# Optimization experiments

Hardware: AMD Instinct MI355X
Metric: run time of the kernel (lower is better)

The kernel has to match this reference:

```python
import jax, jax.numpy as jnp
import numpy as np

NUM_GROUPS = 32
EPS = 1e-5


def group_norm(x, w, b):
    # x: [B,C,H,W], 32 groups
    B, C, H, W = x.shape
    xg = x.reshape(B, NUM_GROUPS, C // NUM_GROUPS, H, W)
    mean = xg.mean(axis=(2, 3, 4), keepdims=True)
    var = xg.var(axis=(2, 3, 4), keepdims=True)
    xn = ((xg - mean) * jax.lax.rsqrt(var + EPS)).reshape(B, C, H, W)
    return xn * w[None, :, None, None] + b[None, :, None, None]


def conv1x1(x, w, b):
    # x: [B,C,H,W], w: [O,C], b: [O]
    return jnp.einsum('bchw,oc->bohw', x, w) + b[None, :, None, None]


def setup_inputs() -> dict:
    key = jax.random.key(0)
    ks = jax.random.split(key, 7)
    B, C, H, W = 16, 512, 32, 32
    x = jax.random.normal(ks[0], (B, C, H, W), dtype=jnp.float32)
    gn_w = jnp.ones((C,), dtype=jnp.float32)
    gn_b = jnp.zeros((C,), dtype=jnp.float32)
    s = 1.0 / np.sqrt(C)
    qkv_w = jax.random.normal(ks[1], (3 * C, C), dtype=jnp.float32) * s
    qkv_b = jnp.zeros((3 * C,), dtype=jnp.float32)
    proj_w = jax.random.normal(ks[2], (C, C), dtype=jnp.float32) * s
    proj_b = jnp.zeros((C,), dtype=jnp.float32)
    return {"x": x, "gn_w": gn_w, "gn_b": gn_b, "qkv_w": qkv_w,
            "qkv_b": qkv_b, "proj_w": proj_w, "proj_b": proj_b}


def reference(x, gn_w, gn_b, qkv_w, qkv_b, proj_w, proj_b):
    B, C, H, W = x.shape
    qkv = conv1x1(group_norm(x, gn_w, gn_b), qkv_w, qkv_b)
    q, k, v = jnp.split(qkv, 3, axis=1)
    scale = (C // 8) ** (-0.5)
    # attn: [B, h, w, H, W]
    attn = jnp.einsum('bchw,bcHW->bhwHW', q * scale, k)
    # NOTE: faithful to original torch code: softmax over the LAST axis only
    attn = jax.nn.softmax(attn, axis=-1)
    out = jnp.einsum('bhwHW,bcHW->bchw', attn, v)
    return x + conv1x1(out, proj_w, proj_b)
```

## Files before the change

### kernel.cpp

```cpp
#include <hip/hip_runtime.h>
#include <hip/hip_bf16.h>

#define B_    16
#define C_    512
#define S_    1024
#define NGRP  32
#define CPG   16

typedef __attribute__((ext_vector_type(8))) short  short8;
typedef __attribute__((ext_vector_type(4))) short  short4v;
typedef __attribute__((ext_vector_type(4))) float  floatx4;

__device__ __forceinline__ unsigned short f2bf(float f) {
    __hip_bfloat16 h = __float2bfloat16(f);
    unsigned short u;
    __builtin_memcpy(&u, &h, 2);
    return u;
}

__global__ __launch_bounds__(256)
void gn_fused_kernel(const float* __restrict__ x, const float* __restrict__ w,
                     const float* __restrict__ bias, __hip_bfloat16* __restrict__ xnT) {
    int bg = blockIdx.x;
    int b = bg >> 5, g = bg & 31;
    const float4* xp = (const float4*)(x + (size_t)bg * (CPG * S_));
    int tid = threadIdx.x;

    float4 vv[16];
    float s = 0.f, ss = 0.f;
#pragma unroll
    for (int r = 0; r < 16; ++r) {
        float4 v = xp[r * 256 + tid];
        vv[r] = v;
        s  += v.x + v.y + v.z + v.w;
        ss += v.x*v.x + v.y*v.y + v.z*v.z + v.w*v.w;
    }
    for (int off = 32; off > 0; off >>= 1) {
        s  += __shfl_down(s, off);
        ss += __shfl_down(ss, off);
    }
    __shared__ float red[2][4];
    __shared__ float msh[2];
    int wid = tid >> 6, lane = tid & 63;
    if (lane == 0) { red[0][wid] = s; red[1][wid] = ss; }
    __syncthreads();
    if (tid == 0) {
        float a = 0.f, c = 0.f;
        for (int i = 0; i < 4; ++i) { a += red[0][i]; c += red[1][i]; }
        float mean = a / (float)(CPG * S_);
        float var  = c / (float)(CPG * S_) - mean * mean;
        msh[0] = mean;
        msh[1] = rsqrtf(var + 1e-5f);
    }
    __syncthreads();
    float mean = msh[0], inv = msh[1];

    float sc[16], sh[16];
#pragma unroll
    for (int c = 0; c < 16; ++c) {
        float wc = w[g * 16 + c];
        sc[c] = inv * wc;
        sh[c] = bias[g * 16 + c] - mean * inv * wc;
    }

#pragma unroll
    for (int kk = 0; kk < 4; ++kk) {
        unsigned short outp[16];
#pragma unroll
        for (int c = 0; c < 16; ++c) {
            float v = (kk == 0) ? vv[c].x : (kk == 1) ? vv[c].y : (kk == 2) ? vv[c].z : vv[c].w;
            outp[c] = f2bf(v * sc[c] + sh[c]);
        }
        int srow = 4 * tid + kk;
        unsigned short* dst = (unsigned short*)xnT + ((size_t)(b * S_ + srow) * C_ + g * 16);
        *(short8*)dst       = *(short8*)outp;
        *(short8*)(dst + 8) = *(short8*)(outp + 8);
    }
}

__global__ __launch_bounds__(256)
void prep_kernel(const float* __restrict__ qkv_w, const float* __restrict__ proj_w,
                 const float* __restrict__ qkv_b,
                 unsigned short* __restrict__ bufX,
                 unsigned short* __restrict__ bufY,
                 float* __restrict__ bqWk, float* __restrict__ biasvp)
{
    int blk = blockIdx.x;
    int tid = threadIdx.x;
    if (blk < 192) {
        __shared__ float T[64][65];
        int mat = blk >> 6, tile = blk & 63;
        int r0 = (tile >> 3) * 64, c0 = (tile & 7) * 64;
        const float* src; unsigned short* dst;
        if (mat == 0)      { src = qkv_w + 512 * 512;  dst = bufX; }
        else if (mat == 1) { src = qkv_w;              dst = bufY; }
        else               { src = qkv_w + 1024 * 512; dst = bufY + 262144; }
#pragma unroll
        for (int rr = 0; rr < 4; ++rr) {
            int sr = rr * 16 + (tid >> 4);
            int sc = (tid & 15) * 4;
            float4 v = *(const float4*)(src + (size_t)(c0 + sr) * 512 + r0 + sc);
            T[sc][sr] = v.x; T[sc + 1][sr] = v.y; T[sc + 2][sr] = v.z; T[sc + 3][sr] = v.w;
        }
        __syncthreads();
#pragma unroll
        for (int rr = 0; rr < 4; ++rr) {
            int dr = rr * 16 + (tid >> 4);
            int dc = (tid & 15) * 4;
            short4v o;
            o[0] = (short)f2bf(T[dr][dc]);     o[1] = (short)f2bf(T[dr][dc + 1]);
            o[2] = (short)f2bf(T[dr][dc + 2]); o[3] = (short)f2bf(T[dr][dc + 3]);
            *(short4v*)(dst + (size_t)(r0 + dr) * 512 + c0 + dc) = o;
        }
    } else if (blk < 256) {
        unsigned short* wp = bufX + 262144;
#pragma unroll
        for (int t = 0; t < 4; ++t) {
            int i = (blk - 192) * 4096 + t * 1024 + tid * 4;
            float4 v = *(const float4*)(proj_w + i);
            short4v o;
            o[0] = (short)f2bf(v.x); o[1] = (short)f2bf(v.y);
            o[2] = (short)f2bf(v.z); o[3] = (short)f2bf(v.w);
            *(short4v*)(wp + i) = o;
        }
    } else if (blk < 264) {
        int sub = blk - 256;
        int j = (sub & 1) * 256 + tid;
        int o0 = (sub >> 1) * 128;
        float acc = 0.f;
#pragma unroll 8
        for (int oo = 0; oo < 128; ++oo) {
            int o = o0 + oo;
            acc += qkv_b[o] * qkv_w[(size_t)(512 + o) * 512 + j];
        }
        atomicAdd(&bqWk[j], acc);
    } else {
        int wv = tid >> 6, lane = tid & 63;
        int c = (blk - 264) * 4 + wv;
        float s = 0.f;
#pragma unroll
        for (int t = 0; t < 8; ++t)
            s += proj_w[(size_t)c * 512 + t * 64 + lane] * qkv_b[1024 + t * 64 + lane];
        for (int off = 32; off > 0; off >>= 1) s += __shfl_down(s, off);
        if (lane == 0) biasvp[c] = s;
    }
}

template<int BIAS_MODE, bool OUT_BF16, bool RESID, bool SWIZ, int KTOT>
__global__ __launch_bounds__(256)
void mfma_gemm(const unsigned short* __restrict__ A, const unsigned short* __restrict__ Bm,
               const float* __restrict__ bias, const float* __restrict__ resid,
               void* __restrict__ Yv,
               int lda, int ldb, int ldy,
               size_t sA, size_t sB, size_t sY, size_t sR, float alpha,
               int ntsh, int nxsh)
{
    __shared__ unsigned short As[2 * 128 * 32];
    __shared__ unsigned short Bs[2 * 128 * 32];
    int bx, by, bz;
    if (SWIZ) {
        int lin = blockIdx.x;
        int xcd = lin & 7, sup = lin >> 3;
        bz = xcd + ((sup >> ntsh) << 3);
        int tile = sup & ((1 << ntsh) - 1);
        bx = tile & ((1 << nxsh) - 1);
        by = tile >> nxsh;
    } else { bx = blockIdx.x; by = blockIdx.y; bz = blockIdx.z; }

    const unsigned short* Ab = A  + (size_t)bz * sA;
    const unsigned short* Bb = Bm + (size_t)bz * sB;
    const int tid = threadIdx.x, wave = tid >> 6, lane = tid & 63;
    const int m0 = by * 128, n0 = bx * 128;
    const int wr = wave >> 1, wc = wave & 1, lr = lane & 15, kq = lane >> 4;
    const int row0 = tid >> 2, kc0 = (tid & 3) << 3;

    floatx4 acc[4][4] = {};

    for (int k0 = 0; k0 < KTOT; k0 += 64) {
        __syncthreads();
#pragma unroll
        for (int kk = 0; kk < 2; ++kk) {
#pragma unroll
            for (int r = 0; r < 2; ++r) {
                const unsigned short* ga = Ab + (size_t)(m0 + r * 64 + row0) * lda + k0 + kk * 32 + kc0;
                __builtin_amdgcn_global_load_lds(
                    (const __attribute__((address_space(1))) void*)ga,
                    (__attribute__((address_space(3))) void*)(As + kk * 4096 + (r * 256 + wave * 64) * 8),
                    16, 0, 0);
                const unsigned short* gb = Bb + (size_t)(n0 + r * 64 + row0) * ldb + k0 + kk * 32 + kc0;
                __builtin_amdgcn_global_load_lds(
                    (const __attribute__((address_space(1))) void*)gb,
                    (__attribute__((address_space(3))) void*)(Bs + kk * 4096 + (r * 256 + wave * 64) * 8),
                    16, 0, 0);
            }
        }
        __syncthreads();

#pragma unroll
        for (int kk = 0; kk < 2; ++kk) {
            short8 af[4], bfr[4];
#pragma unroll
            for (int i = 0; i < 4; ++i)
                af[i] = *(const short8*)&As[kk * 4096 + (wr * 64 + i * 16 + lr) * 32 + kq * 8];
#pragma unroll
            for (int j = 0; j < 4; ++j)
                bfr[j] = *(const short8*)&Bs[kk * 4096 + (wc * 64 + j * 16 + lr) * 32 + kq * 8];
#pragma unroll
            for (int i = 0; i < 4; ++i)
#pragma unroll
                for (int j = 0; j < 4; ++j)
                    acc[i][j] = __builtin_amdgcn_mfma_f32_16x16x32_bf16(af[i], bfr[j], acc[i][j], 0, 0, 0);
        }
    }

    const size_t ybase = (size_t)bz * sY;
    const size_t rbase = (size_t)bz * sR;
#pragma unroll
    for (int i = 0; i < 4; ++i) {
#pragma unroll
        for (int r = 0; r < 4; ++r) {
            int m = m0 + wr * 64 + i * 16 + kq * 4 + r;
            float bm = (BIAS_MODE == 1) ? bias[m] : 0.f;
#pragma unroll
            for (int j = 0; j < 4; ++j) {
                int n = n0 + wc * 64 + j * 16 + lr;
                float vv = acc[i][j][r] * alpha + bm;
                if (BIAS_MODE == 2) vv += bias[n];
                if (RESID) vv += resid[rbase + (size_t)m * ldy + n];
                if (OUT_BF16)
                    ((__hip_bfloat16*)Yv)[ybase + (size_t)m * ldy + n] = __float2bfloat16(vv);
                else
                    ((float*)Yv)[ybase + (size_t)m * ldy + n] = vv;
            }
        }
    }
}

__global__ __launch_bounds__(512)
void scores_softmax8(const unsigned short* __restrict__ A,
                     const unsigned short* __restrict__ Bm,
                     unsigned short* __restrict__ P)
{
    __shared__ __align__(16) unsigned short lds[65536];
    char* asb = (char*)lds;
    char* bsb = (char*)lds + 65536;

    const int bid = blockIdx.x;
    const int bz = bid >> 4, t16 = bid & 15;
    const int by = t16 >> 2, bx = t16 & 3;
    const int m0 = by << 8, n0 = bx << 8;

    const size_t sAB = (size_t)S_ * 512;
    const unsigned short* Ab = A  + (size_t)bz * sAB;
    const unsigned short* Bb = Bm + (size_t)bz * sAB;

    const int tid = threadIdx.x, wave = tid >> 6, lane = tid & 63;
    const int wr = wave >> 2, wc = wave & 3;
    const int lr = lane & 15, kq = lane >> 4;
    const int swz = (lr & 7) << 4;

    floatx4 acc[8][4] = {};
    short8 aF[4][2], bF[2][2][2];

    auto stage = [&](const unsigned short* __restrict__ G, int row0, int t,
                     char* base, int buf, int half) {
#pragma unroll
        for (int c = 0; c < 2; ++c) {
            int x = c * 8192 + tid * 16;
            int row = x >> 7;
            int colb = (x & 127) ^ ((row & 7) << 4);
            const unsigned short* ga = G + (((size_t)(row0 + row)) << 9) + (t << 6) + (colb >> 1);
            char* ldst = base + buf * 32768 + half * 16384 + c * 8192 + wave * 1024;
            __builtin_amdgcn_global_load_lds(
                (const __attribute__((address_space(1))) void*)ga,
                (__attribute__((address_space(3))) void*)ldst, 16, 0, 0);
        }
    };
    auto rdA = [&](int buf, int mh, int ii, int kk) {
        int byte = buf * 32768 + wr * 16384 + (mh * 64 + ii * 16 + lr) * 128
                 + ((kk * 64 + kq * 16) ^ swz);
        return *(const short8*)(asb + byte);
    };
    auto rdB = [&](int buf, int nh, int jj, int kk) {
        int trow = wc * 64 + (nh * 2 + jj) * 16 + lr;
        int byte = buf * 32768 + (trow >> 7) * 16384 + (trow & 127) * 128
                 + ((kk * 64 + kq * 16) ^ swz);
        return *(const short8*)(bsb + byte);
    };

    stage(Ab, m0,       0, asb, 0, 0);
    stage(Bb, n0,       0, bsb, 0, 0);
    stage(Bb, n0 + 128, 0, bsb, 0, 1);
    stage(Ab, m0 + 128, 0, asb, 0, 1);
    stage(Ab, m0,       1, asb, 1, 0);
    stage(Bb, n0,       1, bsb, 1, 0);
    stage(Bb, n0 + 128, 1, bsb, 1, 1);
    asm volatile("s_waitcnt vmcnt(6)" ::: "memory");
    __builtin_amdgcn_s_barrier();

    for (int t = 0; t < 8; ++t) {
        const int buf = t & 1;
#pragma unroll
        for (int ii = 0; ii < 4; ++ii) { aF[ii][0] = rdA(buf, 0, ii, 0); aF[ii][1] = rdA(buf, 0, ii, 1); }
#pragma unroll
        for (int jj = 0; jj < 2; ++jj) { bF[0][jj][0] = rdB(buf, 0, jj, 0); bF[0][jj][1] = rdB(buf, 0, jj, 1); }
        if (t < 7) stage(Ab, m0 + 128, t + 1, asb, (t + 1) & 1, 1);
        __builtin_amdgcn_s_barrier();
        asm volatile("s_waitcnt lgkmcnt(0)" ::: "memory");
        __builtin_amdgcn_s_setprio(1);
#pragma unroll
        for (int ii = 0; ii < 4; ++ii)
#pragma unroll
            for (int jj = 0; jj < 2; ++jj)
#pragma unroll
                for (int kk = 0; kk < 2; ++kk)
                    acc[ii][jj] = __builtin_amdgcn_mfma_f32_16x16x32_bf16(aF[ii][kk], bF[0][jj][kk], acc[ii][jj], 0, 0, 0);
        __builtin_amdgcn_s_setprio(0);
        __builtin_amdgcn_s_barrier();
#pragma unroll
        for (int jj = 0; jj < 2; ++jj) { bF[1][jj][0] = rdB(buf, 1, jj, 0); bF[1][jj][1] = rdB(buf, 1, jj, 1); }
        __builtin_amdgcn_s_barrier();
        asm volatile("s_waitcnt lgkmcnt(0)" ::: "memory");
        __builtin_amdgcn_s_setprio(1);
#pragma unroll
        for (int ii = 0; ii < 4; ++ii)
#pragma unroll
            for (int jj = 0; jj < 2; ++jj)
#pragma unroll
                for (int kk = 0; kk < 2; ++kk)
                    acc[ii][2 + jj] = __builtin_amdgcn_mfma_f32_16x16x32_bf16(aF[ii][kk], bF[1][jj][kk], acc[ii][2 + jj], 0, 0, 0);
        __builtin_amdgcn_s_setprio(0);
        __builtin_amdgcn_s_barrier();
#pragma unroll
        for (int ii = 0; ii < 4; ++ii) { aF[ii][0] = rdA(buf, 1, ii, 0); aF[ii][1] = rdA(buf, 1, ii, 1); }
        if (t < 6) stage(Bb, n0, t + 2, bsb, buf, 0);
        __builtin_amdgcn_s_barrier();
        asm volatile("s_waitcnt lgkmcnt(0)" ::: "memory");
        __builtin_amdgcn_s_setprio(1);
#pragma unroll
        for (int ii = 0; ii < 4; ++ii)
#pragma unroll
            for (int jj = 0; jj < 2; ++jj)
#pragma unroll
                for (int kk = 0; kk < 2; ++kk)
                    acc[4 + ii][2 + jj] = __builtin_amdgcn_mfma_f32_16x16x32_bf16(aF[ii][kk], bF[1][jj][kk], acc[4 + ii][2 + jj], 0, 0, 0);
        __builtin_amdgcn_s_setprio(0);
        __builtin_amdgcn_s_barrier();
        if (t < 6) {
            stage(Ab, m0,       t + 2, asb, buf, 0);
            stage(Bb, n0 + 128, t + 2, bsb, buf, 1);
        }
        __builtin_amdgcn_s_setprio(1);
#pragma unroll
        for (int ii = 0; ii < 4; ++ii)
#pragma unroll
            for (int jj = 0; jj < 2; ++jj)
#pragma unroll
                for (int kk = 0; kk < 2; ++kk)
                    acc[4 + ii][jj] = __builtin_amdgcn_mfma_f32_16x16x32_bf16(aF[ii][kk], bF[0][jj][kk], acc[4 + ii][jj], 0, 0, 0);
        __builtin_amdgcn_s_setprio(0);
        if (t < 6) { asm volatile("s_waitcnt vmcnt(6)" ::: "memory"); }
        else       { asm volatile("s_waitcnt vmcnt(0)" ::: "memory"); }
        __builtin_amdgcn_s_barrier();
    }

#pragma unroll
    for (int j = 0; j < 4; ++j) {
        int sqc = wc * 64 + j * 16 + lr;
        int srow = sqc * 512;
        int sxor = (sqc & 7) << 4;
#pragma unroll
        for (int h = 0; h < 4; ++h) {
            float v0[4], v1[4];
            float mx = -1e30f;
#pragma unroll
            for (int r = 0; r < 4; ++r) {
                v0[r] = acc[2 * h][j][r]     * 0.125f;
                v1[r] = acc[2 * h + 1][j][r] * 0.125f;
                mx = fmaxf(mx, fmaxf(v0[r], v1[r]));
            }
            mx = fmaxf(mx, __shfl_xor(mx, 16));
            mx = fmaxf(mx, __shfl_xor(mx, 32));
            float sm = 0.f;
#pragma unroll
            for (int r = 0; r < 4; ++r) {
                v0[r] = __expf(v0[r] - mx);
                v1[r] = __expf(v1[r] - mx);
                sm += v0[r] + v1[r];
            }
            sm += __shfl_xor(sm, 16);
            sm += __shfl_xor(sm, 32);
            float inv = 1.f / sm;
            short4v p0, p1;
#pragma unroll
            for (int r = 0; r < 4; ++r) {
                p0[r] = (short)f2bf(v0[r] * inv);
                p1[r] = (short)f2bf(v1[r] * inv);
            }
            int kb = (wr * 128 + h * 32 + kq * 4) * 2;
            *(short4v*)(asb + ((srow + kb) ^ sxor))      = p0;
            *(short4v*)(asb + ((srow + kb + 32) ^ sxor)) = p1;
        }
    }
    __syncthreads();

    const size_t pbase = ((size_t)bz << 20) + (size_t)n0 * 1024 + m0;
#pragma unroll
    for (int it = 0; it < 16; ++it) {
        int row = wave * 32 + it * 2 + (lane >> 5);
        int colb = (lane & 31) << 4;
        short8 v = *(const short8*)(asb + ((row * 512 + colb) ^ ((row & 7) << 4)));
        *(short8*)(P + pbase + (size_t)row * 1024 + (colb >> 1)) = v;
    }
}

extern "C" void kernel_launch(void* const* d_in, const int* in_sizes, int n_in,
                              void* d_out, int out_size, void* d_ws, size_t ws_size,
                              hipStream_t stream) {
    const float* x     = (const float*)d_in[0];
    const float* gn_w  = (const float*)d_in[1];
    const float* gn_b  = (const float*)d_in[2];
    const float* qkv_w = (const float*)d_in[3];
    const float* qkv_b = (const float*)d_in[4];
    const float* pr_w  = (const float*)d_in[5];
    const float* pr_b  = (const float*)d_in[6];
    float* out = (float*)d_out;

    char* w = (char*)d_ws;
    __hip_bfloat16* xnT  = (__hip_bfloat16*)w;
    __hip_bfloat16* u    = (__hip_bfloat16*)(w + (16u << 20));
    __hip_bfloat16* Vp   = (__hip_bfloat16*)(w + (32u << 20));
    __hip_bfloat16* P    = (__hip_bfloat16*)(w + (48u << 20));
    unsigned short* bufX = (unsigned short*)(w + (80u << 20));
    unsigned short* bufY = (unsigned short*)(w + (81u << 20));
    unsigned short* bufZ = (unsigned short*)(w + (82u << 20));
    float*          bqWk = (float*)(w + (83u << 20));
    float*          bvp  = (float*)(w + (83u << 20) + 4096);

    hipMemsetAsync(bqWk, 0, 512 * sizeof(float), stream);

    prep_kernel<<<392, 256, 0, stream>>>(qkv_w, pr_w, qkv_b, bufX, bufY, bqWk, bvp);

    gn_fused_kernel<<<B_ * NGRP, 256, 0, stream>>>(x, gn_w, gn_b, xnT);

    mfma_gemm<0, true, false, false, 512><<<dim3(4, 4, 2), 256, 0, stream>>>(
        bufX, bufY, nullptr, nullptr, bufZ,
        512, 512, 512, 262144, 262144, 262144, 0, 1.f, 0, 0);

    mfma_gemm<2, true, false, false, 512><<<dim3(4, 128, 1), 256, 0, stream>>>(
        (const unsigned short*)xnT, bufZ, bqWk, nullptr, u,
        512, 512, 512, 0, 0, 0, 0, 1.f, 0, 0);

    mfma_gemm<1, true, false, true, 512><<<512, 256, 0, stream>>>(
        bufZ + 262144, (const unsigned short*)xnT, bvp, nullptr, Vp,
        512, 512, 1024, 0, (size_t)S_ * 512, (size_t)512 * S_, 0, 1.f, 5, 3);

    scores_softmax8<<<256, 512, 0, stream>>>(
        (const unsigned short*)xnT, (const unsigned short*)u, (unsigned short*)P);

    mfma_gemm<1, false, true, true, 1024><<<512, 256, 0, stream>>>(
        (const unsigned short*)Vp, (const unsigned short*)P, pr_b, x, out,
        1024, 1024, 1024, (size_t)512 * S_, (size_t)S_ * S_, (size_t)512 * S_,
        (size_t)512 * S_, 1.f, 5, 3);
}
```

Baseline: 209.6 us.

## Fuse attention scores, softmax and PV-projection GEMM; merge GN with weight GEMM

```diff
diff --git a/kernel.cpp b/kernel.cpp
--- a/kernel.cpp
+++ b/kernel.cpp
@@ -11,71 +11,15 @@
 typedef __attribute__((ext_vector_type(4))) short  short4v;
 typedef __attribute__((ext_vector_type(4))) float  floatx4;
 
+#define GLOAD16(ga, ld) __builtin_amdgcn_global_load_lds( \
+    (const __attribute__((address_space(1))) void*)(ga),  \
+    (__attribute__((address_space(3))) void*)(ld), 16, 0, 0)
+
 __device__ __forceinline__ unsigned short f2bf(float f) {
     __hip_bfloat16 h = __float2bfloat16(f);
     unsigned short u;
     __builtin_memcpy(&u, &h, 2);
     return u;
-}
-
-__global__ __launch_bounds__(256)
-void gn_fused_kernel(const float* __restrict__ x, const float* __restrict__ w,
-                     const float* __restrict__ bias, __hip_bfloat16* __restrict__ xnT) {
-    int bg = blockIdx.x;
-    int b = bg >> 5, g = bg & 31;
-    const float4* xp = (const float4*)(x + (size_t)bg * (CPG * S_));
-    int tid = threadIdx.x;
-
-    float4 vv[16];
-    float s = 0.f, ss = 0.f;
-#pragma unroll
-    for (int r = 0; r < 16; ++r) {
-        float4 v = xp[r * 256 + tid];
-        vv[r] = v;
-        s  += v.x + v.y + v.z + v.w;
-        ss += v.x*v.x + v.y*v.y + v.z*v.z + v.w*v.w;
-    }
-    for (int off = 32; off > 0; off >>= 1) {
-        s  += __shfl_down(s, off);
-        ss += __shfl_down(ss, off);
-    }
-    __shared__ float red[2][4];
-    __shared__ float msh[2];
-    int wid = tid >> 6, lane = tid & 63;
-    if (lane == 0) { red[0][wid] = s; red[1][wid] = ss; }
-    __syncthreads();
-    if (tid == 0) {
-        float a = 0.f, c = 0.f;
-        for (int i = 0; i < 4; ++i) { a += red[0][i]; c += red[1][i]; }
-        float mean = a / (float)(CPG * S_);
-        float var  = c / (float)(CPG * S_) - mean * mean;
-        msh[0] = mean;
-        msh[1] = rsqrtf(var + 1e-5f);
-    }
-    __syncthreads();
-    float mean = msh[0], inv = msh[1];
-
-    float sc[16], sh[16];
-#pragma unroll
-    for (int c = 0; c < 16; ++c) {
-        float wc = w[g * 16 + c];
-        sc[c] = inv * wc;
-        sh[c] = bias[g * 16 + c] - mean * inv * wc;
-    }
-
-#pragma unroll
-    for (int kk = 0; kk < 4; ++kk) {
-        unsigned short outp[16];
-#pragma unroll
-        for (int c = 0; c < 16; ++c) {
-            float v = (kk == 0) ? vv[c].x : (kk == 1) ? vv[c].y : (kk == 2) ? vv[c].z : vv[c].w;
-            outp[c] = f2bf(v * sc[c] + sh[c]);
-        }
-        int srow = 4 * tid + kk;
-        unsigned short* dst = (unsigned short*)xnT + ((size_t)(b * S_ + srow) * C_ + g * 16);
-        *(short8*)dst       = *(short8*)outp;
-        *(short8*)(dst + 8) = *(short8*)(outp + 8);
-    }
 }
 
 __global__ __launch_bounds__(256)
@@ -146,113 +90,136 @@
     }
 }
 
-template<int BIAS_MODE, bool OUT_BF16, bool RESID, bool SWIZ, int KTOT>
 __global__ __launch_bounds__(256)
-void mfma_gemm(const unsigned short* __restrict__ A, const unsigned short* __restrict__ Bm,
-               const float* __restrict__ bias, const float* __restrict__ resid,
-               void* __restrict__ Yv,
-               int lda, int ldb, int ldy,
-               size_t sA, size_t sB, size_t sY, size_t sR, float alpha,
-               int ntsh, int nxsh)
+void gn_plus_w(const float* __restrict__ x, const float* __restrict__ gnw,
+               const float* __restrict__ gnb, __hip_bfloat16* __restrict__ xnT,
+               const unsigned short* __restrict__ bufX,
+               const unsigned short* __restrict__ bufY,
+               unsigned short* __restrict__ bufZ)
 {
-    __shared__ unsigned short As[2 * 128 * 32];
-    __shared__ unsigned short Bs[2 * 128 * 32];
-    int bx, by, bz;
-    if (SWIZ) {
-        int lin = blockIdx.x;
-        int xcd = lin & 7, sup = lin >> 3;
-        bz = xcd + ((sup >> ntsh) << 3);
-        int tile = sup & ((1 << ntsh) - 1);
-        bx = tile & ((1 << nxsh) - 1);
-        by = tile >> nxsh;
-    } else { bx = blockIdx.x; by = blockIdx.y; bz = blockIdx.z; }
-
-    const unsigned short* Ab = A  + (size_t)bz * sA;
-    const unsigned short* Bb = Bm + (size_t)bz * sB;
-    const int tid = threadIdx.x, wave = tid >> 6, lane = tid & 63;
-    const int m0 = by * 128, n0 = bx * 128;
-    const int wr = wave >> 1, wc = wave & 1, lr = lane & 15, kq = lane >> 4;
-    const int row0 = tid >> 2, kc0 = (tid & 3) << 3;
-
-    floatx4 acc[4][4] = {};
-
-    for (int k0 = 0; k0 < KTOT; k0 += 64) {
+    __shared__ __align__(16) char smem[32832];
+    int blk = blockIdx.x;
+    int tid = threadIdx.x;
+
+    if (blk < 512) {
+        int b = blk >> 5, g = blk & 31;
+        const float4* xp = (const float4*)(x + (size_t)blk * (CPG * S_));
+        float4 vv[16];
+        float s = 0.f, ss = 0.f;
+#pragma unroll
+        for (int r = 0; r < 16; ++r) {
+            float4 v = xp[r * 256 + tid];
+            vv[r] = v;
+            s  += v.x + v.y + v.z + v.w;
+            ss += v.x*v.x + v.y*v.y + v.z*v.z + v.w*v.w;
+        }
+        for (int off = 32; off > 0; off >>= 1) {
+            s  += __shfl_down(s, off);
+            ss += __shfl_down(ss, off);
+        }
+        float* red = (float*)(smem + 32768);
+        float* msh = (float*)(smem + 32800);
+        int wid = tid >> 6, lane = tid & 63;
+        if (lane == 0) { red[wid] = s; red[4 + wid] = ss; }
         __syncthreads();
-#pragma unroll
-        for (int kk = 0; kk < 2; ++kk) {
-#pragma unroll
-            for (int r = 0; r < 2; ++r) {
-                const unsigned short* ga = Ab + (size_t)(m0 + r * 64 + row0) * lda + k0 + kk * 32 + kc0;
-                __builtin_amdgcn_global_load_lds(
-                    (const __attribute__((address_space(1))) void*)ga,
-                    (__attribute__((address_space(3))) void*)(As + kk * 4096 + (r * 256 + wave * 64) * 8),
-                    16, 0, 0);
-                const unsigned short* gb = Bb + (size_t)(n0 + r * 64 + row0) * ldb + k0 + kk * 32 + kc0;
-                __builtin_amdgcn_global_load_lds(
-                    (const __attribute__((address_space(1))) void*)gb,
-                    (__attribute__((address_space(3))) void*)(Bs + kk * 4096 + (r * 256 + wave * 64) * 8),
-                    16, 0, 0);
-            }
+        if (tid == 0) {
+            float a = 0.f, c = 0.f;
+            for (int i = 0; i < 4; ++i) { a += red[i]; c += red[4 + i]; }
+            float mean = a / (float)(CPG * S_);
+            float var  = c / (float)(CPG * S_) - mean * mean;
+            msh[0] = mean;
+            msh[1] = rsqrtf(var + 1e-5f);
         }
         __syncthreads();
-
-#pragma unroll
-        for (int kk = 0; kk < 2; ++kk) {
-            short8 af[4], bfr[4];
-#pragma unroll
-            for (int i = 0; i < 4; ++i)
-                af[i] = *(const short8*)&As[kk * 4096 + (wr * 64 + i * 16 + lr) * 32 + kq * 8];
-#pragma unroll
-            for (int j = 0; j < 4; ++j)
-                bfr[j] = *(const short8*)&Bs[kk * 4096 + (wc * 64 + j * 16 + lr) * 32 + kq * 8];
-#pragma unroll
-            for (int i = 0; i < 4; ++i)
+        float mean = msh[0], inv = msh[1];
+
+        float sc[16], sh[16];
+#pragma unroll
+        for (int c = 0; c < 16; ++c) {
+            float wc = gnw[g * 16 + c];
+            sc[c] = inv * wc;
+            sh[c] = gnb[g * 16 + c] - mean * inv * wc;
+        }
+#pragma unroll
+        for (int kk = 0; kk < 4; ++kk) {
+            unsigned short outp[16];
+#pragma unroll
+            for (int c = 0; c < 16; ++c) {
+                float v = (kk == 0) ? vv[c].x : (kk == 1) ? vv[c].y : (kk == 2) ? vv[c].z : vv[c].w;
+                outp[c] = f2bf(v * sc[c] + sh[c]);
+            }
+            int srow = 4 * tid + kk;
+            unsigned short* dst = (unsigned short*)xnT + ((size_t)(b * S_ + srow) * C_ + g * 16);
+            *(short8*)dst       = *(short8*)outp;
+            *(short8*)(dst + 8) = *(short8*)(outp + 8);
+        }
+    } else {
+        unsigned short* As = (unsigned short*)smem;
+        unsigned short* Bs = (unsigned short*)(smem + 16384);
+        int id = blk - 512;
+        int bx = id & 3, by = (id >> 2) & 3, bz = id >> 4;
+        const unsigned short* Ab = bufX + (size_t)bz * 262144;
+        const unsigned short* Bb = bufY + (size_t)bz * 262144;
+        __hip_bfloat16* Y = (__hip_bfloat16*)bufZ + (size_t)bz * 262144;
+        const int wave = tid >> 6, lane = tid & 63;
+        const int m0 = by * 128, n0 = bx * 128;
+        const int wr = wave >> 1, wc = wave & 1, lr = lane & 15, kq = lane >> 4;
+        const int row0 = tid >> 2, kc0 = (tid & 3) << 3;
+
+        floatx4 acc[4][4] = {};
+        for (int k0 = 0; k0 < 512; k0 += 64) {
+            __syncthreads();
+#pragma unroll
+            for (int kk = 0; kk < 2; ++kk) {
+#pragma unroll
+                for (int r = 0; r < 2; ++r) {
+                    const unsigned short* ga = Ab + (size_t)(m0 + r * 64 + row0) * 512 + k0 + kk * 32 + kc0;
+                    GLOAD16(ga, As + kk * 4096 + (r * 256 + wave * 64) * 8);
+                    const unsigned short* gb = Bb + (size_t)(n0 + r * 64 + row0) * 512 + k0 + kk * 32 + kc0;
+                    GLOAD16(gb, Bs + kk * 4096 + (r * 256 + wave * 64) * 8);
+                }
+            }
+            __syncthreads();
+#pragma unroll
+            for (int kk = 0; kk < 2; ++kk) {
+                short8 af[4], bfr[4];
+#pragma unroll
+                for (int i = 0; i < 4; ++i)
+                    af[i] = *(const short8*)&As[kk * 4096 + (wr * 64 + i * 16 + lr) * 32 + kq * 8];
 #pragma unroll
                 for (int j = 0; j < 4; ++j)
-                    acc[i][j] = __builtin_amdgcn_mfma_f32_16x16x32_bf16(af[i], bfr[j], acc[i][j], 0, 0, 0);
-        }
+                    bfr[j] = *(const short8*)&Bs[kk * 4096 + (wc * 64 + j * 16 + lr) * 32 + kq * 8];
+#pragma unroll
+                for (int i = 0; i < 4; ++i)
+#pragma unroll
+                    for (int j = 0; j < 4; ++j)
+                        acc[i][j] = __builtin_amdgcn_mfma_f32_16x16x32_bf16(af[i], bfr[j], acc[i][j], 0, 0, 0);
+            }
+        }
+#pragma unroll
+        for (int i = 0; i < 4; ++i)
+#pragma unroll
+            for (int r = 0; r < 4; ++r) {
+                int m = m0 + wr * 64 + i * 16 + kq * 4 + r;
+#pragma unroll
+                for (int j = 0; j < 4; ++j) {
+                    int n = n0 + wc * 64 + j * 16 + lr;
+                    Y[(size_t)m * 512 + n] = __float2bfloat16(acc[i][j][r]);
+                }
+            }
     }
-
-    const size_t ybase = (size_t)bz * sY;
-    const size_t rbase = (size_t)bz * sR;
-#pragma unroll
-    for (int i = 0; i < 4; ++i) {
-#pragma unroll
-        for (int r = 0; r < 4; ++r) {
-            int m = m0 + wr * 64 + i * 16 + kq * 4 + r;
-            float bm = (BIAS_MODE == 1) ? bias[m] : 0.f;
-#pragma unroll
-            for (int j = 0; j < 4; ++j) {
-                int n = n0 + wc * 64 + j * 16 + lr;
-                float vv = acc[i][j][r] * alpha + bm;
-                if (BIAS_MODE == 2) vv += bias[n];
-                if (RESID) vv += resid[rbase + (size_t)m * ldy + n];
-                if (OUT_BF16)
-                    ((__hip_bfloat16*)Yv)[ybase + (size_t)m * ldy + n] = __float2bfloat16(vv);
-                else
-                    ((float*)Yv)[ybase + (size_t)m * ldy + n] = vv;
-            }
-        }
-    }
-}
-
-__global__ __launch_bounds__(512)
-void scores_softmax8(const unsigned short* __restrict__ A,
-                     const unsigned short* __restrict__ Bm,
-                     unsigned short* __restrict__ P)
+}
+
+template<int BIAS_MODE>
+__device__ __forceinline__
+void gemm256_body(char* lds, const unsigned short* __restrict__ Ab,
+                  const unsigned short* __restrict__ Bb,
+                  const float* __restrict__ bias,
+                  __hip_bfloat16* __restrict__ Y,
+                  int ldy, size_t ybase, int m0, int n0)
 {
-    __shared__ __align__(16) unsigned short lds[65536];
-    char* asb = (char*)lds;
-    char* bsb = (char*)lds + 65536;
-
-    const int bid = blockIdx.x;
-    const int bz = bid >> 4, t16 = bid & 15;
-    const int by = t16 >> 2, bx = t16 & 3;
-    const int m0 = by << 8, n0 = bx << 8;
-
-    const size_t sAB = (size_t)S_ * 512;
-    const unsigned short* Ab = A  + (size_t)bz * sAB;
-    const unsigned short* Bb = Bm + (size_t)bz * sAB;
+    char* asb = lds;
+    char* bsb = lds + 65536;
 
     const int tid = threadIdx.x, wave = tid >> 6, lane = tid & 63;
     const int wr = wave >> 2, wc = wave & 3;
@@ -270,10 +237,7 @@
             int row = x >> 7;
             int colb = (x & 127) ^ ((row & 7) << 4);
             const unsigned short* ga = G + (((size_t)(row0 + row)) << 9) + (t << 6) + (colb >> 1);
-            char* ldst = base + buf * 32768 + half * 16384 + c * 8192 + wave * 1024;
-            __builtin_amdgcn_global_load_lds(
-                (const __attribute__((address_space(1))) void*)ga,
-                (__attribute__((address_space(3))) void*)ldst, 16, 0, 0);
+            GLOAD16(ga, base + buf * 32768 + half * 16384 + c * 8192 + wave * 1024);
         }
     };
     auto rdA = [&](int buf, int mh, int ii, int kk) {
@@ -365,53 +329,217 @@
     }
 
 #pragma unroll
-    for (int j = 0; j < 4; ++j) {
-        int sqc = wc * 64 + j * 16 + lr;
-        int srow = sqc * 512;
-        int sxor = (sqc & 7) << 4;
-#pragma unroll
-        for (int h = 0; h < 4; ++h) {
-            float v0[4], v1[4];
-            float mx = -1e30f;
-#pragma unroll
-            for (int r = 0; r < 4; ++r) {
-                v0[r] = acc[2 * h][j][r]     * 0.125f;
-                v1[r] = acc[2 * h + 1][j][r] * 0.125f;
-                mx = fmaxf(mx, fmaxf(v0[r], v1[r]));
-            }
-            mx = fmaxf(mx, __shfl_xor(mx, 16));
-            mx = fmaxf(mx, __shfl_xor(mx, 32));
-            float sm = 0.f;
-#pragma unroll
-            for (int r = 0; r < 4; ++r) {
-                v0[r] = __expf(v0[r] - mx);
-                v1[r] = __expf(v1[r] - mx);
-                sm += v0[r] + v1[r];
-            }
-            sm += __shfl_xor(sm, 16);
-            sm += __shfl_xor(sm, 32);
-            float inv = 1.f / sm;
-            short4v p0, p1;
-#pragma unroll
-            for (int r = 0; r < 4; ++r) {
-                p0[r] = (short)f2bf(v0[r] * inv);
-                p1[r] = (short)f2bf(v1[r] * inv);
-            }
-            int kb = (wr * 128 + h * 32 + kq * 4) * 2;
-            *(short4v*)(asb + ((srow + kb) ^ sxor))      = p0;
-            *(short4v*)(asb + ((srow + kb + 32) ^ sxor)) = p1;
-        }
+    for (int idx = 0; idx < 8; ++idx)
+#pragma unroll
+        for (int r = 0; r < 4; ++r) {
+            int m = m0 + wr * 128 + idx * 16 + kq * 4 + r;
+            float bm = (BIAS_MODE == 1) ? bias[m] : 0.f;
+#pragma unroll
+            for (int j = 0; j < 4; ++j) {
+                int n = n0 + wc * 64 + j * 16 + lr;
+                float vv = acc[idx][j][r] + bm;
+                if (BIAS_MODE == 2) vv += bias[n];
+                Y[ybase + (size_t)m * ldy + n] = __float2bfloat16(vv);
+            }
+        }
+}
+
+__global__ __launch_bounds__(512)
+void fused_s45(const unsigned short* __restrict__ xnT,
+               const unsigned short* __restrict__ bufZ,
+               const float* __restrict__ bqWk, const float* __restrict__ bvp,
+               __hip_bfloat16* __restrict__ u, __hip_bfloat16* __restrict__ Vp)
+{
+    __shared__ __align__(16) char lds[131072];
+    int blk = blockIdx.x;
+    if (blk < 128) {
+        int by = blk >> 1, bx = blk & 1;
+        gemm256_body<2>(lds, xnT, bufZ, bqWk, u, 512, 0, by * 256, bx * 256);
+    } else {
+        int lin = blk - 128;
+        int xcd = lin & 7, sup = lin >> 3;
+        int bz = xcd + ((sup >> 3) << 3);
+        int tile = sup & 7;
+        int bx = tile & 3, by = tile >> 2;
+        gemm256_body<1>(lds, bufZ + 262144, xnT + (size_t)bz * ((size_t)S_ * 512),
+                        bvp, Vp, 1024, (size_t)bz * 512 * S_, by * 256, bx * 256);
     }
-    __syncthreads();
-
-    const size_t pbase = ((size_t)bz << 20) + (size_t)n0 * 1024 + m0;
-#pragma unroll
-    for (int it = 0; it < 16; ++it) {
-        int row = wave * 32 + it * 2 + (lane >> 5);
-        int colb = (lane & 31) << 4;
-        short8 v = *(const short8*)(asb + ((row * 512 + colb) ^ ((row & 7) << 4)));
-        *(short8*)(P + pbase + (size_t)row * 1024 + (colb >> 1)) = v;
+}
+
+__global__ __launch_bounds__(512)
+void attn_fused(const unsigned short* __restrict__ xnT,
+                const unsigned short* __restrict__ u,
+                const unsigned short* __restrict__ Vp,
+                const float* __restrict__ prb,
+                const float* __restrict__ x,
+                float* __restrict__ out)
+{
+    __shared__ __align__(16) char lds[147456];
+
+    const int lin = blockIdx.x;
+    const int xcd = lin & 7, sup = lin >> 3;
+    const int bz = xcd + ((sup >> 4) << 3);
+    const int sq0 = (sup & 15) << 6;
+
+    const unsigned short* xb = xnT + (size_t)bz * ((size_t)S_ * 512);
+    const unsigned short* ub = u   + (size_t)bz * ((size_t)S_ * 512);
+    const unsigned short* vb = Vp  + (size_t)bz * ((size_t)512 * S_);
+
+    const int tid = threadIdx.x, wave = tid >> 6, lane = tid & 63;
+    const int lr = lane & 15, kq = lane >> 4;
+    const int kh = wave >> 2, sx = wave & 3;
+    const int ch = wave >> 1, sh = wave & 1;
+    const int swz = (lr & 7) << 4;
+
+    short8 uF[8][2];
+#pragma unroll
+    for (int s = 0; s < 8; ++s)
+#pragma unroll
+        for (int kk = 0; kk < 2; ++kk)
+            uF[s][kk] = *(const short8*)(ub + (size_t)(sq0 + sx * 16 + lr) * 512
+                                            + s * 64 + kk * 32 + kq * 8);
+
+    floatx4 oAcc[8][2] = {};
+
+    auto stage_keys = [&](int kt, int s, int buf) {
+#pragma unroll
+        for (int c = 0; c < 2; ++c) {
+            int xo = c * 8192 + tid * 16;
+            int row = xo >> 7;
+            int colb = (xo & 127) ^ ((row & 7) << 4);
+            const unsigned short* ga = xb + (size_t)(kt * 128 + row) * 512 + s * 64 + (colb >> 1);
+            GLOAD16(ga, lds + buf * 16384 + c * 8192 + wave * 1024);
+        }
+    };
+    auto stage_vp = [&](int kt, int h2, int c8, bool toH1) {
+        int xo = tid * 16;
+        int row = c8 * 64 + (xo >> 7);
+        int colb = (xo & 127) ^ ((row & 7) << 4);
+        const unsigned short* ga = vb + (size_t)row * 1024 + kt * 128 + h2 * 64 + (colb >> 1);
+        int base = toH1 ? ((c8 < 4 ? 0 : 65536) + c8 * 8192) : (32768 + c8 * 8192);
+        GLOAD16(ga, lds + base + wave * 1024);
+    };
+
+    for (int kt = 0; kt < 8; ++kt) {
+        floatx4 sAcc[4] = {};
+        stage_keys(kt, 0, 0);
+        stage_keys(kt, 1, 1);
+        asm volatile("s_waitcnt vmcnt(2)" ::: "memory");
+        __builtin_amdgcn_s_barrier();
+#pragma unroll
+        for (int s = 0; s < 8; ++s) {
+            const int buf = s & 1;
+            short8 aF[4][2];
+#pragma unroll
+            for (int i = 0; i < 4; ++i)
+#pragma unroll
+                for (int kk = 0; kk < 2; ++kk)
+                    aF[i][kk] = *(const short8*)(lds + buf * 16384
+                        + (kh * 64 + i * 16 + lr) * 128 + ((kk * 64 + kq * 16) ^ swz));
+            asm volatile("s_waitcnt lgkmcnt(0)" ::: "memory");
+            __builtin_amdgcn_s_barrier();
+            if (s < 6) stage_keys(kt, s + 2, buf);
+            stage_vp(kt, 0, s, false);
+            __builtin_amdgcn_s_setprio(1);
+#pragma unroll
+            for (int i = 0; i < 4; ++i)
+#pragma unroll
+                for (int kk = 0; kk < 2; ++kk)
+                    sAcc[i] = __builtin_amdgcn_mfma_f32_16x16x32_bf16(aF[i][kk], uF[s][kk], sAcc[i], 0, 0, 0);
+            __builtin_amdgcn_s_setprio(0);
+            if (s == 0)      { asm volatile("s_waitcnt vmcnt(3)" ::: "memory"); }
+            else if (s < 6)  { asm volatile("s_waitcnt vmcnt(4)" ::: "memory"); }
+            else if (s == 6) { asm volatile("s_waitcnt vmcnt(2)" ::: "memory"); }
+            __builtin_amdgcn_s_barrier();
+        }
+
+#pragma unroll
+        for (int c8 = 0; c8 < 8; ++c8) stage_vp(kt, 1, c8, true);
+        {
+            const int prow = sx * 16 + lr;
+            const int sxor = (prow & 7) << 4;
+#pragma unroll
+            for (int h = 0; h < 2; ++h) {
+                float v0[4], v1[4];
+                float mx = -1e30f;
+#pragma unroll
+                for (int r = 0; r < 4; ++r) {
+                    v0[r] = sAcc[2 * h][r]     * 0.125f;
+                    v1[r] = sAcc[2 * h + 1][r] * 0.125f;
+                    mx = fmaxf(mx, fmaxf(v0[r], v1[r]));
+                }
+                mx = fmaxf(mx, __shfl_xor(mx, 16));
+                mx = fmaxf(mx, __shfl_xor(mx, 32));
+                float sm = 0.f;
+#pragma unroll
+                for (int r = 0; r < 4; ++r) {
+                    v0[r] = __expf(v0[r] - mx);
+                    v1[r] = __expf(v1[r] - mx);
+                    sm += v0[r] + v1[r];
+                }
+                sm += __shfl_xor(sm, 16);
+                sm += __shfl_xor(sm, 32);
+                float inv = 1.f / sm;
+                short4v p0, p1;
+#pragma unroll
+                for (int r = 0; r < 4; ++r) {
+                    p0[r] = (short)f2bf(v0[r] * inv);
+                    p1[r] = (short)f2bf(v1[r] * inv);
+                }
+                int kb = prow * 256 + kh * 128 + h * 64 + kq * 8;
+                *(short4v*)(lds + 131072 + (kb ^ sxor))        = p0;
+                *(short4v*)(lds + 131072 + ((kb + 32) ^ sxor)) = p1;
+            }
+        }
+        asm volatile("s_waitcnt lgkmcnt(0)" ::: "memory");
+        asm volatile("s_waitcnt vmcnt(8)" ::: "memory");
+        __builtin_amdgcn_s_barrier();
+
+#pragma unroll
+        for (int h2 = 0; h2 < 2; ++h2) {
+            short8 bPF[2][2];
+#pragma unroll
+            for (int j = 0; j < 2; ++j)
+#pragma unroll
+                for (int kk = 0; kk < 2; ++kk) {
+                    int row2 = sh * 32 + j * 16 + lr;
+                    int byte = row2 * 256 + ((h2 * 128 + kk * 64 + kq * 16) ^ ((row2 & 7) << 4));
+                    bPF[j][kk] = *(const short8*)(lds + 131072 + byte);
+                }
+            const int abase = h2 ? (ch < 2 ? 0 : 65536) : 32768;
+            __builtin_amdgcn_s_setprio(1);
+#pragma unroll
+            for (int i = 0; i < 8; ++i) {
+                int row = ch * 128 + i * 16 + lr;
+                short8 a0 = *(const short8*)(lds + abase + row * 128 + ((kq * 16) ^ swz));
+                short8 a1 = *(const short8*)(lds + abase + row * 128 + ((64 + kq * 16) ^ swz));
+#pragma unroll
+                for (int j = 0; j < 2; ++j) {
+                    oAcc[i][j] = __builtin_amdgcn_mfma_f32_16x16x32_bf16(a0, bPF[j][0], oAcc[i][j], 0, 0, 0);
+                    oAcc[i][j] = __builtin_amdgcn_mfma_f32_16x16x32_bf16(a1, bPF[j][1], oAcc[i][j], 0, 0, 0);
+                }
+            }
+            __builtin_amdgcn_s_setprio(0);
+            asm volatile("s_waitcnt lgkmcnt(0)" ::: "memory");
+            if (h2 == 0) { asm volatile("s_waitcnt vmcnt(0)" ::: "memory"); }
+            __builtin_amdgcn_s_barrier();
+        }
     }
+
+    const size_t ob = (size_t)bz * 512 * 1024;
+#pragma unroll
+    for (int i = 0; i < 8; ++i)
+#pragma unroll
+        for (int r = 0; r < 4; ++r) {
+            int m = ch * 128 + i * 16 + kq * 4 + r;
+            float bm = prb[m];
+#pragma unroll
+            for (int j = 0; j < 2; ++j) {
+                int n = sq0 + sh * 32 + j * 16 + lr;
+                size_t idx = ob + (size_t)m * 1024 + n;
+                out[idx] = oAcc[i][j][r] + bm + x[idx];
+            }
+        }
 }
 
 extern "C" void kernel_launch(void* const* d_in, const int* in_sizes, int n_in,
@@ -430,7 +558,6 @@
     __hip_bfloat16* xnT  = (__hip_bfloat16*)w;
     __hip_bfloat16* u    = (__hip_bfloat16*)(w + (16u << 20));
     __hip_bfloat16* Vp   = (__hip_bfloat16*)(w + (32u << 20));
-    __hip_bfloat16* P    = (__hip_bfloat16*)(w + (48u << 20));
     unsigned short* bufX = (unsigned short*)(w + (80u << 20));
     unsigned short* bufY = (unsigned short*)(w + (81u << 20));
     unsigned short* bufZ = (unsigned short*)(w + (82u << 20));
@@ -441,25 +568,12 @@
 
     prep_kernel<<<392, 256, 0, stream>>>(qkv_w, pr_w, qkv_b, bufX, bufY, bqWk, bvp);
 
-    gn_fused_kernel<<<B_ * NGRP, 256, 0, stream>>>(x, gn_w, gn_b, xnT);
-
-    mfma_gemm<0, true, false, false, 512><<<dim3(4, 4, 2), 256, 0, stream>>>(
-        bufX, bufY, nullptr, nullptr, bufZ,
-        512, 512, 512, 262144, 262144, 262144, 0, 1.f, 0, 0);
-
-    mfma_gemm<2, true, false, false, 512><<<dim3(4, 128, 1), 256, 0, stream>>>(
-        (const unsigned short*)xnT, bufZ, bqWk, nullptr, u,
-        512, 512, 512, 0, 0, 0, 0, 1.f, 0, 0);
-
-    mfma_gemm<1, true, false, true, 512><<<512, 256, 0, stream>>>(
-        bufZ + 262144, (const unsigned short*)xnT, bvp, nullptr, Vp,
-        512, 512, 1024, 0, (size_t)S_ * 512, (size_t)512 * S_, 0, 1.f, 5, 3);
-
-    scores_softmax8<<<256, 512, 0, stream>>>(
-        (const unsigned short*)xnT, (const unsigned short*)u, (unsigned short*)P);
-
-    mfma_gemm<1, false, true, true, 1024><<<512, 256, 0, stream>>>(
-        (const unsigned short*)Vp, (const unsigned short*)P, pr_b, x, out,
-        1024, 1024, 1024, (size_t)512 * S_, (size_t)S_ * S_, (size_t)512 * S_,
-        (size_t)512 * S_, 1.f, 5, 3);
-}
+    gn_plus_w<<<544, 256, 0, stream>>>(x, gn_w, gn_b, xnT, bufX, bufY, bufZ);
+
+    fused_s45<<<256, 512, 0, stream>>>((const unsigned short*)xnT, bufZ, bqWk, bvp,
+                                       u, Vp);
+
+    attn_fused<<<256, 512, 0, stream>>>(
+        (const unsigned short*)xnT, (const unsigned short*)u,
+        (const unsigned short*)Vp, pr_b, x, out);
+}
```

Result: faster. 192.6 us (-8.1%).
